# Kernel tuning notes

Hardware: AMD Instinct MI355X
Metric: run time of the kernel (lower is better)

## Reference

```python
import jax, jax.numpy as jnp
import numpy as np

B, N, D = 8, 2048, 512


def setup_inputs() -> dict:
    key = jax.random.key(0)
    ks = jax.random.split(key, 8)
    s = 1.0 / np.sqrt(D)
    return {
        "x": jax.random.normal(ks[0], (B, N, D), dtype=jnp.float32),
        "event_lengths": jax.random.randint(ks[1], (B,), 1, N + 1, dtype=jnp.int64),
        "Wq": jax.random.uniform(ks[2], (D, D), jnp.float32, -s, s),
        "bq": jnp.zeros((D,), jnp.float32),
        "Wk": jax.random.uniform(ks[3], (D, D), jnp.float32, -s, s),
        "bk": jnp.zeros((D,), jnp.float32),
        "Wv": jax.random.uniform(ks[4], (D, D), jnp.float32, -s, s),
        "bv": jnp.zeros((D,), jnp.float32),
    }


def reference(x, event_lengths, Wq, bq, Wk, bk, Wv, bv):
    # x: [B, N, D]; linear layers follow torch convention y = x @ W^T + b
    q = jnp.einsum("bnd,ed->bne", x, Wq) + bq
    k = jnp.einsum("bnd,ed->bne", x, Wk) + bk
    v = jnp.einsum("bnd,ed->bne", x, Wv) + bv

    d = x.shape[-1]
    scores = jnp.einsum("bqd,bkd->bqk", q, k) / jnp.sqrt(jnp.asarray(d, jnp.float32))

    # per-sample padding mask: valid iff row < len AND col < len
    n = x.shape[1]
    idx = jnp.arange(n)
    L = event_lengths[:, None, None]  # [B,1,1]
    mask = (idx[None, :, None] < L) & (idx[None, None, :] < L)  # [B,N,N]
    scores = jnp.where(mask, scores, jnp.float32(-1e9))

    attn = jax.nn.softmax(scores, axis=-1)  # dropout omitted (eval mode)
    return jnp.einsum("bqk,bkd->bqd", attn, v)
```

## Files before the change

kernel.cpp:

```cpp
#include <hip/hip_runtime.h>

typedef _Float16 half8 __attribute__((ext_vector_type(8)));
typedef _Float16 half4 __attribute__((ext_vector_type(4)));
typedef float    floatx4 __attribute__((ext_vector_type(4)));
typedef float    float4v __attribute__((ext_vector_type(4)));

#define BB 8
#define NN 2048
#define DD 512


__device__ __forceinline__ void stage_tile(const _Float16* __restrict__ g,
                                           int gstride, _Float16* lds,
                                           int w, int lane)
{
#pragma unroll
    for (int j = 0; j < 2; ++j) {
        int grp = w * 2 + j;
        int r   = grp * 16 + (lane >> 2);
        int cb  = (lane & 3) ^ ((r >> 1) & 3);
        const _Float16* gp = g + (size_t)r * gstride + cb * 8;
        _Float16* lp = lds + grp * 512;
        __builtin_amdgcn_global_load_lds(
            (const __attribute__((address_space(1))) void*)gp,
            (__attribute__((address_space(3))) void*)lp, 16, 0, 0);
    }
}

__device__ __forceinline__ void stage_tile64(const _Float16* __restrict__ g,
                                             int gstride, _Float16* lds,
                                             int w, int lane)
{
    int r  = w * 16 + (lane >> 2);
    int cb = (lane & 3) ^ ((r >> 1) & 3);
    const _Float16* gp = g + (size_t)r * gstride + cb * 8;
    _Float16* lp = lds + w * 512;
    __builtin_amdgcn_global_load_lds(
        (const __attribute__((address_space(1))) void*)gp,
        (__attribute__((address_space(3))) void*)lp, 16, 0, 0);
}

__device__ __forceinline__ half8 frag(const _Float16* tile, int m, int quad)
{
    return *(const half8*)&tile[m * 32 + ((quad ^ ((m >> 1) & 3)) * 8)];
}

__global__ __launch_bounds__(256) void prep_kernel(
    const float* __restrict__ x, const float* __restrict__ Wq,
    const float* __restrict__ Wk, const float* __restrict__ Wv,
    const int* __restrict__ lens,
    _Float16* __restrict__ xh, _Float16* __restrict__ wqh,
    _Float16* __restrict__ wkh, _Float16* __restrict__ wvh)
{
    const int XQ = (BB * NN * DD) / 4;
    const int WQ = (DD * DD) / 4;
    int t = blockIdx.x * 256 + threadIdx.x;
    const float* src; _Float16* dst; int i;
    if (t < XQ) {
        int row = t >> 7;
        int b   = row >> 11;
        if ((row & 2047) >= ((lens[b] + 127) & ~127)) return;
        src = x;  dst = xh;  i = t;
    }
    else if (t < XQ + WQ)   { src = Wq; dst = wqh; i = t - XQ; }
    else if (t < XQ + 2*WQ) { src = Wk; dst = wkh; i = t - XQ - WQ; }
    else if (t < XQ + 3*WQ) { src = Wv; dst = wvh; i = t - XQ - 2*WQ; }
    else return;
    float4v f = *(const float4v*)&src[(size_t)i * 4];
    half4 h;
    for (int j = 0; j < 4; ++j) h[j] = (_Float16)f[j];
    *(half4*)&dst[(size_t)i * 4] = h;
}

__global__ __launch_bounds__(256) void meanx_kernel(
    const float* __restrict__ x, float* __restrict__ sx)
{
    const int b  = blockIdx.y;
    const int n0 = blockIdx.x * 64;
    const int d0 = threadIdx.x;
    float s0 = 0.f, s1 = 0.f;
    const float* base = x + ((size_t)b * NN + n0) * DD;
    for (int n = 0; n < 64; ++n) {
        s0 += base[n * DD + d0];
        s1 += base[n * DD + d0 + 256];
    }
    atomicAdd(&sx[b * DD + d0], s0);
    atomicAdd(&sx[b * DD + d0 + 256], s1);
}

__global__ __launch_bounds__(256) void mvgemv_kernel(
    const float* __restrict__ Wv, const float* __restrict__ bv,
    const float* __restrict__ sx, float* __restrict__ mean_v)
{
    const int blk = blockIdx.x;
    const int b   = blk >> 7;
    const int e   = (blk & 127) * 4 + (threadIdx.x >> 6);
    const int lane = threadIdx.x & 63;
    const float* wr = Wv + (size_t)e * DD + lane * 8;
    const float* xr = sx + b * DD + lane * 8;
    float s = 0.f;
    for (int j = 0; j < 8; ++j) s += wr[j] * xr[j];
    for (int off = 32; off > 0; off >>= 1) s += __shfl_xor(s, off);
    if (lane == 0)
        mean_v[b * DD + e] = s * (1.0f / 2048.0f) + bv[e];
}

__global__ __launch_bounds__(256) void projqk_kernel(
    const _Float16* __restrict__ xh,
    const _Float16* __restrict__ wqh, const _Float16* __restrict__ wkh,
    const float* __restrict__ bq, const float* __restrict__ bk,
    const int* __restrict__ lens,
    _Float16* __restrict__ qb, _Float16* __restrict__ kb)
{
    const int z = blockIdx.z;
    const int r0 = blockIdx.y * 128;
    const int bb = r0 >> 11;
    if ((r0 & 2047) >= lens[bb]) return;
    const _Float16* Wh  = z ? wkh : wqh;
    const float*    bias= z ? bk  : bq;
    _Float16*       outp= z ? kb  : qb;
    const int c0 = blockIdx.x * 128;

    __shared__ __align__(16) _Float16 As[128 * 32];
    __shared__ __align__(16) _Float16 Bs[128 * 32];

    const int tid  = threadIdx.x;
    const int lane = tid & 63;
    const int w    = tid >> 6;
    const int wm   = w >> 1, wn = w & 1;
    const int lr   = lane & 15;
    const int quad = lane >> 4;

    floatx4 zero; zero[0]=0.f; zero[1]=0.f; zero[2]=0.f; zero[3]=0.f;
    floatx4 acc[4][4];
    for (int i = 0; i < 4; ++i)
        for (int j = 0; j < 4; ++j) acc[i][j] = zero;

    for (int kt = 0; kt < DD / 32; ++kt) {
        __syncthreads();
        stage_tile(xh + (size_t)r0 * DD + kt * 32, DD, As, w, lane);
        stage_tile(Wh + (size_t)c0 * DD + kt * 32, DD, Bs, w, lane);
        __syncthreads();
        half8 a[4], b[4];
        for (int mt = 0; mt < 4; ++mt) a[mt] = frag(As, wm * 64 + mt * 16 + lr, quad);
        for (int nt = 0; nt < 4; ++nt) b[nt] = frag(Bs, wn * 64 + nt * 16 + lr, quad);
        for (int mt = 0; mt < 4; ++mt)
            for (int nt = 0; nt < 4; ++nt)
                acc[mt][nt] = __builtin_amdgcn_mfma_f32_16x16x32_f16(a[mt], b[nt], acc[mt][nt], 0, 0, 0);
    }

    for (int mt = 0; mt < 4; ++mt)
        for (int nt = 0; nt < 4; ++nt)
            for (int r = 0; r < 4; ++r) {
                int row = r0 + wm * 64 + mt * 16 + quad * 4 + r;
                int col = c0 + wn * 64 + nt * 16 + lr;
                outp[(size_t)row * DD + col] = (_Float16)(acc[mt][nt][r] + bias[col]);
            }
}

__global__ __launch_bounds__(256) void projv_kernel(
    const _Float16* __restrict__ xh,
    const _Float16* __restrict__ wvh, const float* __restrict__ bv,
    const int* __restrict__ lens, _Float16* __restrict__ vhT)
{
    const int b  = blockIdx.z;
    const int e0 = blockIdx.y * 128;
    const int n0 = blockIdx.x * 128;
    if (n0 >= lens[b]) return;

    __shared__ __align__(16) _Float16 As[128 * 32];
    __shared__ __align__(16) _Float16 Bs[128 * 32];

    const int tid  = threadIdx.x;
    const int lane = tid & 63;
    const int w    = tid >> 6;
    const int wm   = w >> 1, wn = w & 1;
    const int lr   = lane & 15;
    const int quad = lane >> 4;

    floatx4 zero; zero[0]=0.f; zero[1]=0.f; zero[2]=0.f; zero[3]=0.f;
    floatx4 acc[4][4];
    for (int i = 0; i < 4; ++i)
        for (int j = 0; j < 4; ++j) acc[i][j] = zero;

    for (int kt = 0; kt < DD / 32; ++kt) {
        __syncthreads();
        stage_tile(wvh + (size_t)e0 * DD + kt * 32, DD, As, w, lane);
        stage_tile(xh + ((size_t)b * NN + n0) * DD + kt * 32, DD, Bs, w, lane);
        __syncthreads();
        half8 a[4], bfr[4];
        for (int mt = 0; mt < 4; ++mt) a[mt]   = frag(As, wm * 64 + mt * 16 + lr, quad);
        for (int nt = 0; nt < 4; ++nt) bfr[nt] = frag(Bs, wn * 64 + nt * 16 + lr, quad);
        for (int mt = 0; mt < 4; ++mt)
            for (int nt = 0; nt < 4; ++nt)
                acc[mt][nt] = __builtin_amdgcn_mfma_f32_16x16x32_f16(a[mt], bfr[nt], acc[mt][nt], 0, 0, 0);
    }

    for (int mt = 0; mt < 4; ++mt)
        for (int nt = 0; nt < 4; ++nt)
            for (int r = 0; r < 4; ++r) {
                int e = e0 + wm * 64 + mt * 16 + quad * 4 + r;
                int n = n0 + wn * 64 + nt * 16 + lr;
                vhT[((size_t)b * DD + e) * NN + n] = (_Float16)(acc[mt][nt][r] + bv[e]);
            }
}

__global__ __launch_bounds__(256) void scores_kernel(
    const _Float16* __restrict__ qb, const _Float16* __restrict__ kb,
    const int* __restrict__ lens, _Float16* __restrict__ S)
{
    const int b  = blockIdx.z;
    const int r0 = blockIdx.y * 128;
    const int c0 = blockIdx.x * 128;
    const int L  = lens[b];
    if (r0 >= L || c0 >= L) return;
    const _Float16* A  = qb + (size_t)b * NN * DD;
    const _Float16* Bm = kb + (size_t)b * NN * DD;

    __shared__ __align__(16) _Float16 As[128 * 32];
    __shared__ __align__(16) _Float16 Bs[128 * 32];

    const int tid  = threadIdx.x;
    const int lane = tid & 63;
    const int w    = tid >> 6;
    const int wm   = w >> 1, wn = w & 1;
    const int lr   = lane & 15;
    const int quad = lane >> 4;

    floatx4 zero; zero[0]=0.f; zero[1]=0.f; zero[2]=0.f; zero[3]=0.f;
    floatx4 acc[4][4];
    for (int i = 0; i < 4; ++i)
        for (int j = 0; j < 4; ++j) acc[i][j] = zero;

    for (int kt = 0; kt < DD / 32; ++kt) {
        __syncthreads();
        stage_tile(A  + (size_t)r0 * DD + kt * 32, DD, As, w, lane);
        stage_tile(Bm + (size_t)c0 * DD + kt * 32, DD, Bs, w, lane);
        __syncthreads();
        half8 a[4], bfr[4];
        for (int mt = 0; mt < 4; ++mt) a[mt]   = frag(As, wm * 64 + mt * 16 + lr, quad);
        for (int nt = 0; nt < 4; ++nt) bfr[nt] = frag(Bs, wn * 64 + nt * 16 + lr, quad);
        for (int mt = 0; mt < 4; ++mt)
            for (int nt = 0; nt < 4; ++nt)
                acc[mt][nt] = __builtin_amdgcn_mfma_f32_16x16x32_f16(a[mt], bfr[nt], acc[mt][nt], 0, 0, 0);
    }

    const float scale = 0.044194173824159216f;
    for (int mt = 0; mt < 4; ++mt)
        for (int nt = 0; nt < 4; ++nt)
            for (int r = 0; r < 4; ++r) {
                int q    = r0 + wm * 64 + mt * 16 + quad * 4 + r;
                int kcol = c0 + wn * 64 + nt * 16 + lr;
                S[((size_t)b * NN + q) * NN + kcol] = (_Float16)(acc[mt][nt][r] * scale);
            }
}

__global__ __launch_bounds__(256) void softmax_kernel(
    _Float16* __restrict__ S, const int* __restrict__ lens)
{
    const int b = blockIdx.y, q = blockIdx.x;
    const int L = lens[b];
    if (q >= L) return;
    const int Lp32 = (L + 31) & ~31;
    const size_t base = ((size_t)b * NN + q) * NN;
    const int tid  = threadIdx.x;
    const int lane = tid & 63;
    const int w    = tid >> 6;
    const int k0   = tid * 8;
    const bool active = k0 < Lp32;
    const float NEG = -__builtin_huge_valf();

    float f[8];
    if (active) {
        half8 v = *(const half8*)&S[base + k0];
        for (int j = 0; j < 8; ++j) f[j] = (k0 + j < L) ? (float)v[j] : NEG;
    } else {
        for (int j = 0; j < 8; ++j) f[j] = NEG;
    }

    float m = f[0];
    for (int j = 1; j < 8; ++j) m = fmaxf(m, f[j]);
    for (int off = 32; off > 0; off >>= 1) m = fmaxf(m, __shfl_xor(m, off));
    __shared__ float redm[4];
    __shared__ float reds[4];
    if (lane == 0) redm[w] = m;
    __syncthreads();
    m = fmaxf(fmaxf(redm[0], redm[1]), fmaxf(redm[2], redm[3]));

    float e[8], s = 0.f;
    for (int j = 0; j < 8; ++j) { e[j] = __expf(f[j] - m); s += e[j]; }
    for (int off = 32; off > 0; off >>= 1) s += __shfl_xor(s, off);
    if (lane == 0) reds[w] = s;
    __syncthreads();
    s = (reds[0] + reds[1]) + (reds[2] + reds[3]);

    float inv = 1.0f / s;
    if (active) {
        half8 o;
        for (int j = 0; j < 8; ++j) o[j] = (_Float16)(e[j] * inv);
        *(half8*)&S[base + k0] = o;
    }
}

__global__ __launch_bounds__(256) void pv_kernel(
    const _Float16* __restrict__ P, const _Float16* __restrict__ vhT,
    const int* __restrict__ lens, const float* __restrict__ mean_v,
    float* __restrict__ out)
{
    const int b  = blockIdx.z;
    const int L  = lens[b];
    const int r0 = blockIdx.y * 64;
    const int c0 = blockIdx.x * 128;
    const int KT = (r0 < L) ? ((L + 31) >> 5) : 0;
    const _Float16* A  = P   + (size_t)b * NN * NN;
    const _Float16* Vh = vhT + (size_t)b * DD * NN;

    __shared__ __align__(16) _Float16 As[2][64 * 32];
    __shared__ __align__(16) _Float16 Bhs[2][128 * 32];

    const int tid  = threadIdx.x;
    const int lane = tid & 63;
    const int w    = tid >> 6;
    const int lr   = lane & 15;
    const int quad = lane >> 4;

    floatx4 zero; zero[0]=0.f; zero[1]=0.f; zero[2]=0.f; zero[3]=0.f;
    floatx4 acc[4][2];
    for (int i = 0; i < 4; ++i)
        for (int j = 0; j < 2; ++j) acc[i][j] = zero;

    if (KT > 0) {
        stage_tile64(A + (size_t)r0 * NN, NN, As[0], w, lane);
        stage_tile (Vh + (size_t)c0 * NN, NN, Bhs[0], w, lane);
    }
    for (int kt = 0; kt < KT; ++kt) {
        const int cur = kt & 1;
        __syncthreads();
        if (kt + 1 < KT) {
            stage_tile64(A + (size_t)r0 * NN + (kt + 1) * 32, NN, As[cur ^ 1], w, lane);
            stage_tile (Vh + (size_t)c0 * NN + (kt + 1) * 32, NN, Bhs[cur ^ 1], w, lane);
        }
        half8 a[4], bh[2];
        for (int mt = 0; mt < 4; ++mt) a[mt]  = frag(As[cur], mt * 16 + lr, quad);
        for (int nt = 0; nt < 2; ++nt) bh[nt] = frag(Bhs[cur], w * 32 + nt * 16 + lr, quad);
        for (int mt = 0; mt < 4; ++mt)
            for (int nt = 0; nt < 2; ++nt)
                acc[mt][nt] = __builtin_amdgcn_mfma_f32_16x16x32_f16(a[mt], bh[nt], acc[mt][nt], 0, 0, 0);
    }

    float mval[2];
    for (int nt = 0; nt < 2; ++nt)
        mval[nt] = mean_v[b * DD + c0 + w * 32 + nt * 16 + lr];

    for (int mt = 0; mt < 4; ++mt)
        for (int nt = 0; nt < 2; ++nt)
            for (int r = 0; r < 4; ++r) {
                int q = r0 + mt * 16 + quad * 4 + r;
                int e = c0 + w * 32 + nt * 16 + lr;
                float val = (q < L) ? acc[mt][nt][r] : mval[nt];
                out[((size_t)b * NN + q) * DD + e] = val;
            }
}

extern "C" void kernel_launch(void* const* d_in, const int* in_sizes, int n_in,
                              void* d_out, int out_size, void* d_ws, size_t ws_size,
                              hipStream_t stream) {
    const float* x    = (const float*)d_in[0];
    const int*   lens = (const int*)d_in[1];
    const float* Wq   = (const float*)d_in[2];
    const float* bq   = (const float*)d_in[3];
    const float* Wk   = (const float*)d_in[4];
    const float* bk   = (const float*)d_in[5];
    const float* Wv   = (const float*)d_in[6];
    const float* bv   = (const float*)d_in[7];
    float* out = (float*)d_out;

    char* ws = (char*)d_ws;
    const size_t MB = 1024 * 1024;
    _Float16* qb  = (_Float16*)(ws);
    _Float16* kb  = (_Float16*)(ws + 16 * MB);
    _Float16* vh  = (_Float16*)(ws + 32 * MB);
    float*    mv  = (float*)   (ws + 48 * MB);
    float*    sx  = (float*)   (ws + 48 * MB + 64 * 1024);
    _Float16* S   = (_Float16*)(ws + 64 * MB);
    _Float16* xh  = (_Float16*)(ws + 64 * MB);
    _Float16* wqh = (_Float16*)(ws + 80 * MB);
    _Float16* wkh = (_Float16*)(ws + 80 * MB + 512 * 1024);
    _Float16* wvh = (_Float16*)(ws + 81 * MB);

    hipMemsetAsync(sx, 0, BB * DD * sizeof(float), stream);
    prep_kernel  <<<8960, 256, 0, stream>>>(x, Wq, Wk, Wv, lens, xh, wqh, wkh, wvh);
    meanx_kernel <<<dim3(32, 8),     256, 0, stream>>>(x, sx);
    mvgemv_kernel<<<1024,            256, 0, stream>>>(Wv, bv, sx, mv);
    projqk_kernel<<<dim3(4, 128, 2), 256, 0, stream>>>(xh, wqh, wkh, bq, bk, lens, qb, kb);
    projv_kernel <<<dim3(16, 4, 8),  256, 0, stream>>>(xh, wvh, bv, lens, vh);
    scores_kernel<<<dim3(16, 16, 8), 256, 0, stream>>>(qb, kb, lens, S);
    softmax_kernel<<<dim3(2048, 8),  256, 0, stream>>>(S, lens);
    pv_kernel    <<<dim3(4, 32, 8),  256, 0, stream>>>(S, vh, lens, mv, out);
}
```

Baseline: 213.2 us.

## Fuse x conversion with mean reduction and load GEMM fragments directly from global

```diff
diff --git a/kernel.cpp b/kernel.cpp
--- a/kernel.cpp
+++ b/kernel.cpp
@@ -1,91 +1,63 @@
 #include <hip/hip_runtime.h>
 
-typedef _Float16 half8 __attribute__((ext_vector_type(8)));
-typedef _Float16 half4 __attribute__((ext_vector_type(4)));
+typedef _Float16 half8  __attribute__((ext_vector_type(8)));
+typedef _Float16 half4  __attribute__((ext_vector_type(4)));
+typedef _Float16 half2v __attribute__((ext_vector_type(2)));
 typedef float    floatx4 __attribute__((ext_vector_type(4)));
 typedef float    float4v __attribute__((ext_vector_type(4)));
+typedef float    float2v __attribute__((ext_vector_type(2)));
 
 #define BB 8
 #define NN 2048
 #define DD 512
 
-
-__device__ __forceinline__ void stage_tile(const _Float16* __restrict__ g,
-                                           int gstride, _Float16* lds,
-                                           int w, int lane)
-{
-#pragma unroll
-    for (int j = 0; j < 2; ++j) {
-        int grp = w * 2 + j;
-        int r   = grp * 16 + (lane >> 2);
-        int cb  = (lane & 3) ^ ((r >> 1) & 3);
-        const _Float16* gp = g + (size_t)r * gstride + cb * 8;
-        _Float16* lp = lds + grp * 512;
-        __builtin_amdgcn_global_load_lds(
-            (const __attribute__((address_space(1))) void*)gp,
-            (__attribute__((address_space(3))) void*)lp, 16, 0, 0);
-    }
-}
-
-__device__ __forceinline__ void stage_tile64(const _Float16* __restrict__ g,
-                                             int gstride, _Float16* lds,
-                                             int w, int lane)
-{
-    int r  = w * 16 + (lane >> 2);
-    int cb = (lane & 3) ^ ((r >> 1) & 3);
-    const _Float16* gp = g + (size_t)r * gstride + cb * 8;
-    _Float16* lp = lds + w * 512;
-    __builtin_amdgcn_global_load_lds(
-        (const __attribute__((address_space(1))) void*)gp,
-        (__attribute__((address_space(3))) void*)lp, 16, 0, 0);
-}
-
-__device__ __forceinline__ half8 frag(const _Float16* tile, int m, int quad)
-{
-    return *(const half8*)&tile[m * 32 + ((quad ^ ((m >> 1) & 3)) * 8)];
-}
 
 __global__ __launch_bounds__(256) void prep_kernel(
     const float* __restrict__ x, const float* __restrict__ Wq,
     const float* __restrict__ Wk, const float* __restrict__ Wv,
     const int* __restrict__ lens,
     _Float16* __restrict__ xh, _Float16* __restrict__ wqh,
-    _Float16* __restrict__ wkh, _Float16* __restrict__ wvh)
-{
-    const int XQ = (BB * NN * DD) / 4;
-    const int WQ = (DD * DD) / 4;
-    int t = blockIdx.x * 256 + threadIdx.x;
-    const float* src; _Float16* dst; int i;
-    if (t < XQ) {
-        int row = t >> 7;
-        int b   = row >> 11;
-        if ((row & 2047) >= ((lens[b] + 127) & ~127)) return;
-        src = x;  dst = xh;  i = t;
-    }
-    else if (t < XQ + WQ)   { src = Wq; dst = wqh; i = t - XQ; }
-    else if (t < XQ + 2*WQ) { src = Wk; dst = wkh; i = t - XQ - WQ; }
-    else if (t < XQ + 3*WQ) { src = Wv; dst = wvh; i = t - XQ - 2*WQ; }
-    else return;
-    float4v f = *(const float4v*)&src[(size_t)i * 4];
-    half4 h;
-    for (int j = 0; j < 4; ++j) h[j] = (_Float16)f[j];
-    *(half4*)&dst[(size_t)i * 4] = h;
-}
-
-__global__ __launch_bounds__(256) void meanx_kernel(
-    const float* __restrict__ x, float* __restrict__ sx)
+    _Float16* __restrict__ wkh, _Float16* __restrict__ wvh,
+    float* __restrict__ sx)
 {
     const int b  = blockIdx.y;
     const int n0 = blockIdx.x * 64;
-    const int d0 = threadIdx.x;
+    const int t  = threadIdx.x;
+    const int Lp = (lens[b] + 127) & ~127;
+    const float*   base  = x  + ((size_t)b * NN + n0) * DD + 2 * t;
+    _Float16*      hbase = xh + ((size_t)b * NN + n0) * DD + 2 * t;
+
+    int nw = Lp - n0;
+    nw = nw < 0 ? 0 : (nw > 64 ? 64 : nw);
+
     float s0 = 0.f, s1 = 0.f;
-    const float* base = x + ((size_t)b * NN + n0) * DD;
-    for (int n = 0; n < 64; ++n) {
-        s0 += base[n * DD + d0];
-        s1 += base[n * DD + d0 + 256];
-    }
-    atomicAdd(&sx[b * DD + d0], s0);
-    atomicAdd(&sx[b * DD + d0 + 256], s1);
+    int n = 0;
+    for (; n < nw; ++n) {
+        float2v f = *(const float2v*)&base[(size_t)n * DD];
+        s0 += f[0]; s1 += f[1];
+        half2v h; h[0] = (_Float16)f[0]; h[1] = (_Float16)f[1];
+        *(half2v*)&hbase[(size_t)n * DD] = h;
+    }
+    for (; n < 64; ++n) {
+        float2v f = *(const float2v*)&base[(size_t)n * DD];
+        s0 += f[0]; s1 += f[1];
+    }
+    atomicAdd(&sx[b * DD + 2 * t],     s0);
+    atomicAdd(&sx[b * DD + 2 * t + 1], s1);
+
+    const int gbid = b * 32 + blockIdx.x;
+#pragma unroll
+    for (int k = 0; k < 3; ++k) {
+        int wi = gbid * 768 + k * 256 + t;
+        const float* src; _Float16* dst; int i;
+        if (wi < 65536)       { src = Wq; dst = wqh; i = wi; }
+        else if (wi < 131072) { src = Wk; dst = wkh; i = wi - 65536; }
+        else                  { src = Wv; dst = wvh; i = wi - 131072; }
+        float4v f = *(const float4v*)&src[(size_t)i * 4];
+        half4 h;
+        for (int j = 0; j < 4; ++j) h[j] = (_Float16)f[j];
+        *(half4*)&dst[(size_t)i * 4] = h;
+    }
 }
 
 __global__ __launch_bounds__(256) void mvgemv_kernel(
@@ -105,6 +77,48 @@
         mean_v[b * DD + e] = s * (1.0f / 2048.0f) + bv[e];
 }
 
+__device__ __forceinline__ void g128_load(
+    const _Float16* __restrict__ A, const _Float16* __restrict__ B,
+    const int* ao, const int* bo, int kk, half8 a[4], half8 bf[4])
+{
+#pragma unroll
+    for (int i = 0; i < 4; ++i) a[i]  = *(const half8*)(A + ao[i] + kk * 32);
+#pragma unroll
+    for (int i = 0; i < 4; ++i) bf[i] = *(const half8*)(B + bo[i] + kk * 32);
+}
+
+__device__ __forceinline__ void g128_mf(
+    const half8 a[4], const half8 bf[4], floatx4 acc[4][4])
+{
+#pragma unroll
+    for (int mt = 0; mt < 4; ++mt)
+#pragma unroll
+        for (int nt = 0; nt < 4; ++nt)
+            acc[mt][nt] = __builtin_amdgcn_mfma_f32_16x16x32_f16(
+                a[mt], bf[nt], acc[mt][nt], 0, 0, 0);
+}
+
+__device__ __forceinline__ void gemm128(
+    const _Float16* __restrict__ Abase, const _Float16* __restrict__ Bbase,
+    floatx4 acc[4][4], int wm, int wn, int lr, int quad)
+{
+    int ao[4], bo[4];
+#pragma unroll
+    for (int i = 0; i < 4; ++i) {
+        ao[i] = (wm * 64 + i * 16 + lr) * DD + quad * 8;
+        bo[i] = (wn * 64 + i * 16 + lr) * DD + quad * 8;
+    }
+    half8 a0[4], b0[4], a1[4], b1[4];
+    g128_load(Abase, Bbase, ao, bo, 0, a0, b0);
+    for (int k2 = 0; k2 < 8; ++k2) {
+        g128_load(Abase, Bbase, ao, bo, 2 * k2 + 1, a1, b1);
+        g128_mf(a0, b0, acc);
+        int kn = 2 * k2 + 2; if (kn > 15) kn = 15;
+        g128_load(Abase, Bbase, ao, bo, kn, a0, b0);
+        g128_mf(a1, b1, acc);
+    }
+}
+
 __global__ __launch_bounds__(256) void projqk_kernel(
     const _Float16* __restrict__ xh,
     const _Float16* __restrict__ wqh, const _Float16* __restrict__ wkh,
@@ -121,9 +135,6 @@
     _Float16*       outp= z ? kb  : qb;
     const int c0 = blockIdx.x * 128;
 
-    __shared__ __align__(16) _Float16 As[128 * 32];
-    __shared__ __align__(16) _Float16 Bs[128 * 32];
-
     const int tid  = threadIdx.x;
     const int lane = tid & 63;
     const int w    = tid >> 6;
@@ -136,18 +147,7 @@
     for (int i = 0; i < 4; ++i)
         for (int j = 0; j < 4; ++j) acc[i][j] = zero;
 
-    for (int kt = 0; kt < DD / 32; ++kt) {
-        __syncthreads();
-        stage_tile(xh + (size_t)r0 * DD + kt * 32, DD, As, w, lane);
-        stage_tile(Wh + (size_t)c0 * DD + kt * 32, DD, Bs, w, lane);
-        __syncthreads();
-        half8 a[4], b[4];
-        for (int mt = 0; mt < 4; ++mt) a[mt] = frag(As, wm * 64 + mt * 16 + lr, quad);
-        for (int nt = 0; nt < 4; ++nt) b[nt] = frag(Bs, wn * 64 + nt * 16 + lr, quad);
-        for (int mt = 0; mt < 4; ++mt)
-            for (int nt = 0; nt < 4; ++nt)
-                acc[mt][nt] = __builtin_amdgcn_mfma_f32_16x16x32_f16(a[mt], b[nt], acc[mt][nt], 0, 0, 0);
-    }
+    gemm128(xh + (size_t)r0 * DD, Wh + (size_t)c0 * DD, acc, wm, wn, lr, quad);
 
     for (int mt = 0; mt < 4; ++mt)
         for (int nt = 0; nt < 4; ++nt)
@@ -168,9 +168,6 @@
     const int n0 = blockIdx.x * 128;
     if (n0 >= lens[b]) return;
 
-    __shared__ __align__(16) _Float16 As[128 * 32];
-    __shared__ __align__(16) _Float16 Bs[128 * 32];
-
     const int tid  = threadIdx.x;
     const int lane = tid & 63;
     const int w    = tid >> 6;
@@ -183,18 +180,8 @@
     for (int i = 0; i < 4; ++i)
         for (int j = 0; j < 4; ++j) acc[i][j] = zero;
 
-    for (int kt = 0; kt < DD / 32; ++kt) {
-        __syncthreads();
-        stage_tile(wvh + (size_t)e0 * DD + kt * 32, DD, As, w, lane);
-        stage_tile(xh + ((size_t)b * NN + n0) * DD + kt * 32, DD, Bs, w, lane);
-        __syncthreads();
-        half8 a[4], bfr[4];
-        for (int mt = 0; mt < 4; ++mt) a[mt]   = frag(As, wm * 64 + mt * 16 + lr, quad);
-        for (int nt = 0; nt < 4; ++nt) bfr[nt] = frag(Bs, wn * 64 + nt * 16 + lr, quad);
-        for (int mt = 0; mt < 4; ++mt)
-            for (int nt = 0; nt < 4; ++nt)
-                acc[mt][nt] = __builtin_amdgcn_mfma_f32_16x16x32_f16(a[mt], bfr[nt], acc[mt][nt], 0, 0, 0);
-    }
+    gemm128(wvh + (size_t)e0 * DD, xh + ((size_t)b * NN + n0) * DD,
+            acc, wm, wn, lr, quad);
 
     for (int mt = 0; mt < 4; ++mt)
         for (int nt = 0; nt < 4; ++nt)
@@ -214,11 +201,6 @@
     const int c0 = blockIdx.x * 128;
     const int L  = lens[b];
     if (r0 >= L || c0 >= L) return;
-    const _Float16* A  = qb + (size_t)b * NN * DD;
-    const _Float16* Bm = kb + (size_t)b * NN * DD;
-
-    __shared__ __align__(16) _Float16 As[128 * 32];
-    __shared__ __align__(16) _Float16 Bs[128 * 32];
 
     const int tid  = threadIdx.x;
     const int lane = tid & 63;
@@ -232,18 +214,9 @@
     for (int i = 0; i < 4; ++i)
         for (int j = 0; j < 4; ++j) acc[i][j] = zero;
 
-    for (int kt = 0; kt < DD / 32; ++kt) {
-        __syncthreads();
-        stage_tile(A  + (size_t)r0 * DD + kt * 32, DD, As, w, lane);
-        stage_tile(Bm + (size_t)c0 * DD + kt * 32, DD, Bs, w, lane);
-        __syncthreads();
-        half8 a[4], bfr[4];
-        for (int mt = 0; mt < 4; ++mt) a[mt]   = frag(As, wm * 64 + mt * 16 + lr, quad);
-        for (int nt = 0; nt < 4; ++nt) bfr[nt] = frag(Bs, wn * 64 + nt * 16 + lr, quad);
-        for (int mt = 0; mt < 4; ++mt)
-            for (int nt = 0; nt < 4; ++nt)
-                acc[mt][nt] = __builtin_amdgcn_mfma_f32_16x16x32_f16(a[mt], bfr[nt], acc[mt][nt], 0, 0, 0);
-    }
+    gemm128(qb + (size_t)b * NN * DD + (size_t)r0 * DD,
+            kb + (size_t)b * NN * DD + (size_t)c0 * DD,
+            acc, wm, wn, lr, quad);
 
     const float scale = 0.044194173824159216f;
     for (int mt = 0; mt < 4; ++mt)
@@ -302,6 +275,29 @@
     }
 }
 
+__device__ __forceinline__ void pv_load(
+    const _Float16* __restrict__ Pb, const _Float16* __restrict__ Vb,
+    const size_t* aoff, const size_t* boff, int kk, half8 A[4], half8 B[2])
+{
+#pragma unroll
+    for (int mt = 0; mt < 4; ++mt)
+        A[mt] = *(const half8*)(Pb + aoff[mt] + (size_t)kk * 32);
+#pragma unroll
+    for (int nt = 0; nt < 2; ++nt)
+        B[nt] = *(const half8*)(Vb + boff[nt] + (size_t)kk * 32);
+}
+
+__device__ __forceinline__ void pv_mf(
+    const half8 A[4], const half8 B[2], floatx4 acc[4][2])
+{
+#pragma unroll
+    for (int mt = 0; mt < 4; ++mt)
+#pragma unroll
+        for (int nt = 0; nt < 2; ++nt)
+            acc[mt][nt] = __builtin_amdgcn_mfma_f32_16x16x32_f16(
+                A[mt], B[nt], acc[mt][nt], 0, 0, 0);
+}
+
 __global__ __launch_bounds__(256) void pv_kernel(
     const _Float16* __restrict__ P, const _Float16* __restrict__ vhT,
     const int* __restrict__ lens, const float* __restrict__ mean_v,
@@ -312,11 +308,6 @@
     const int r0 = blockIdx.y * 64;
     const int c0 = blockIdx.x * 128;
     const int KT = (r0 < L) ? ((L + 31) >> 5) : 0;
-    const _Float16* A  = P   + (size_t)b * NN * NN;
-    const _Float16* Vh = vhT + (size_t)b * DD * NN;
-
-    __shared__ __align__(16) _Float16 As[2][64 * 32];
-    __shared__ __align__(16) _Float16 Bhs[2][128 * 32];
 
     const int tid  = threadIdx.x;
     const int lane = tid & 63;
@@ -324,28 +315,41 @@
     const int lr   = lane & 15;
     const int quad = lane >> 4;
 
+    const _Float16* Pb = P   + (size_t)b * NN * NN;
+    const _Float16* Vb = vhT + (size_t)b * DD * NN;
+
+    size_t aoff[4], boff[2];
+#pragma unroll
+    for (int mt = 0; mt < 4; ++mt)
+        aoff[mt] = (size_t)(r0 + mt * 16 + lr) * NN + quad * 8;
+#pragma unroll
+    for (int nt = 0; nt < 2; ++nt)
+        boff[nt] = (size_t)(c0 + w * 32 + nt * 16 + lr) * NN + quad * 8;
+
     floatx4 zero; zero[0]=0.f; zero[1]=0.f; zero[2]=0.f; zero[3]=0.f;
     floatx4 acc[4][2];
     for (int i = 0; i < 4; ++i)
         for (int j = 0; j < 2; ++j) acc[i][j] = zero;
 
     if (KT > 0) {
-        stage_tile64(A + (size_t)r0 * NN, NN, As[0], w, lane);
-        stage_tile (Vh + (size_t)c0 * NN, NN, Bhs[0], w, lane);
-    }
-    for (int kt = 0; kt < KT; ++kt) {
-        const int cur = kt & 1;
-        __syncthreads();
-        if (kt + 1 < KT) {
-            stage_tile64(A + (size_t)r0 * NN + (kt + 1) * 32, NN, As[cur ^ 1], w, lane);
-            stage_tile (Vh + (size_t)c0 * NN + (kt + 1) * 32, NN, Bhs[cur ^ 1], w, lane);
+        half8 A0[4], A1[4], A2[4], B0[2], B1[2], B2[2];
+        pv_load(Pb, Vb, aoff, boff, 0, A0, B0);
+        pv_load(Pb, Vb, aoff, boff, KT > 1 ? 1 : 0, A1, B1);
+        int kt = 0;
+        while (true) {
+            int kp = kt + 2 < KT ? kt + 2 : KT - 1;
+            pv_load(Pb, Vb, aoff, boff, kp, A2, B2);
+            pv_mf(A0, B0, acc);
+            if (++kt == KT) break;
+            kp = kt + 2 < KT ? kt + 2 : KT - 1;
+            pv_load(Pb, Vb, aoff, boff, kp, A0, B0);
+            pv_mf(A1, B1, acc);
+            if (++kt == KT) break;
+            kp = kt + 2 < KT ? kt + 2 : KT - 1;
+            pv_load(Pb, Vb, aoff, boff, kp, A1, B1);
+            pv_mf(A2, B2, acc);
+            if (++kt == KT) break;
         }
-        half8 a[4], bh[2];
-        for (int mt = 0; mt < 4; ++mt) a[mt]  = frag(As[cur], mt * 16 + lr, quad);
-        for (int nt = 0; nt < 2; ++nt) bh[nt] = frag(Bhs[cur], w * 32 + nt * 16 + lr, quad);
-        for (int mt = 0; mt < 4; ++mt)
-            for (int nt = 0; nt < 2; ++nt)
-                acc[mt][nt] = __builtin_amdgcn_mfma_f32_16x16x32_f16(a[mt], bh[nt], acc[mt][nt], 0, 0, 0);
     }
 
     float mval[2];
@@ -389,8 +393,7 @@
     _Float16* wvh = (_Float16*)(ws + 81 * MB);
 
     hipMemsetAsync(sx, 0, BB * DD * sizeof(float), stream);
-    prep_kernel  <<<8960, 256, 0, stream>>>(x, Wq, Wk, Wv, lens, xh, wqh, wkh, wvh);
-    meanx_kernel <<<dim3(32, 8),     256, 0, stream>>>(x, sx);
+    prep_kernel  <<<dim3(32, 8),     256, 0, stream>>>(x, Wq, Wk, Wv, lens, xh, wqh, wkh, wvh, sx);
     mvgemv_kernel<<<1024,            256, 0, stream>>>(Wv, bv, sx, mv);
     projqk_kernel<<<dim3(4, 128, 2), 256, 0, stream>>>(xh, wqh, wkh, bq, bk, lens, qb, kb);
     projv_kernel <<<dim3(16, 4, 8),  256, 0, stream>>>(xh, wvh, bv, lens, vh);
```

Result: slower. 394.9 us (+85.3%).
